# Kernel tuning notes

Measured on AMD Instinct MI355X. Metric: run time of the kernel, lower is better.

Reference implementation:

```python
import jax, jax.numpy as jnp
import numpy as np

N_NODES = 50000
N_EDGES = 600000
VOCAB = 1140
EMB = 10
IN1 = 45   # 35 raw feats + 10 embedding
OUT1 = 128
OUT2 = 64
HID = 32   # LSTM hidden, bidirectional -> 64


def setup_inputs() -> dict:
    key = jax.random.key(0)
    ks = jax.random.split(key, 32)

    def lin(k, out_f, in_f):
        kw, _ = jax.random.split(k)
        return jax.random.normal(kw, (out_f, in_f), jnp.float32) / np.sqrt(in_f), jnp.zeros((out_f,), jnp.float32)

    src = jax.random.randint(ks[0], (N_EDGES,), 0, N_NODES)
    dst = jax.random.randint(ks[1], (N_EDGES,), 0, N_NODES)
    x = jax.random.normal(ks[2], (N_NODES, 35), jnp.float32)
    node_id = jax.random.randint(ks[3], (N_NODES,), 0, VOCAB)

    emb = jax.random.normal(ks[4], (VOCAB, EMB), jnp.float32)
    # dgl GraphConv weights are (in, out)
    convW1 = jax.random.normal(ks[5], (IN1, OUT1), jnp.float32) / np.sqrt(IN1)
    convb1 = jnp.zeros((OUT1,), jnp.float32)
    convW2 = jax.random.normal(ks[6], (OUT1, OUT2), jnp.float32) / np.sqrt(OUT1)
    convb2 = jnp.zeros((OUT2,), jnp.float32)
    bn1g = jnp.ones((OUT1,), jnp.float32); bn1b = jnp.zeros((OUT1,), jnp.float32)
    bn2g = jnp.ones((OUT2,), jnp.float32); bn2b = jnp.zeros((OUT2,), jnp.float32)
    bn3g = jnp.ones((OUT2,), jnp.float32); bn3b = jnp.zeros((OUT2,), jnp.float32)
    sc1W, sc1b = lin(ks[7], OUT1, IN1)
    sc2W, sc2b = lin(ks[8], OUT2, OUT1)
    sc3W, sc3b = lin(ks[9], OUT2, OUT2)
    # torch LSTM layout: W_ih (4H, in), W_hh (4H, H), gate order i,f,g,o
    Wih_f = jax.random.normal(ks[10], (4 * HID, OUT2), jnp.float32) / np.sqrt(OUT2)
    Whh_f = jax.random.normal(ks[11], (4 * HID, HID), jnp.float32) / np.sqrt(HID)
    bih_f = jnp.zeros((4 * HID,), jnp.float32); bhh_f = jnp.zeros((4 * HID,), jnp.float32)
    Wih_b = jax.random.normal(ks[12], (4 * HID, OUT2), jnp.float32) / np.sqrt(OUT2)
    Whh_b = jax.random.normal(ks[13], (4 * HID, HID), jnp.float32) / np.sqrt(HID)
    bih_b = jnp.zeros((4 * HID,), jnp.float32); bhh_b = jnp.zeros((4 * HID,), jnp.float32)
    a1W, a1b = lin(ks[14], OUT2, OUT2)
    a2W, a2b = lin(ks[15], 1, OUT2)
    c1W, c1b = lin(ks[16], OUT2, OUT2)
    c2W, c2b = lin(ks[17], 1, OUT2)

    return dict(src=src, dst=dst, x=x, node_id=node_id, emb=emb,
                convW1=convW1, convb1=convb1, convW2=convW2, convb2=convb2,
                bn1g=bn1g, bn1b=bn1b, bn2g=bn2g, bn2b=bn2b, bn3g=bn3g, bn3b=bn3b,
                sc1W=sc1W, sc1b=sc1b, sc2W=sc2W, sc2b=sc2b, sc3W=sc3W, sc3b=sc3b,
                Wih_f=Wih_f, Whh_f=Whh_f, bih_f=bih_f, bhh_f=bhh_f,
                Wih_b=Wih_b, Whh_b=Whh_b, bih_b=bih_b, bhh_b=bhh_b,
                a1W=a1W, a1b=a1b, a2W=a2W, a2b=a2b, c1W=c1W, c1b=c1b, c2W=c2W, c2b=c2b)


def _lstm_dir(seq, Wih, Whh, bih, bhh):
    # seq: [N, in]; unbatched torch LSTM semantics, one direction
    H = Whh.shape[1]
    pre = seq @ Wih.T + bih + bhh  # [N, 4H], input projection hoisted out of scan

    def step(carry, pt):
        h, c = carry
        g4 = pt + h @ Whh.T
        i, f, g, o = jnp.split(g4, 4)
        i = jax.nn.sigmoid(i); f = jax.nn.sigmoid(f)
        g = jnp.tanh(g); o = jax.nn.sigmoid(o)
        c2 = f * c + i * g
        h2 = o * jnp.tanh(c2)
        return (h2, c2), h2

    init = (jnp.zeros((H,), seq.dtype), jnp.zeros((H,), seq.dtype))
    _, hs = jax.lax.scan(step, init, pre)
    return hs  # [N, H]


def reference(src, dst, x, node_id, emb,
              convW1, convb1, convW2, convb2,
              bn1g, bn1b, bn2g, bn2b, bn3g, bn3b,
              sc1W, sc1b, sc2W, sc2b, sc3W, sc3b,
              Wih_f, Whh_f, bih_f, bhh_f, Wih_b, Whh_b, bih_b, bhh_b,
              a1W, a1b, a2W, a2b, c1W, c1b, c2W, c2b):
    N = x.shape[0]
    # dgl.add_self_loop
    loops = jnp.arange(N)
    s = jnp.concatenate([src, loops])
    d = jnp.concatenate([dst, loops])
    ones = jnp.ones(s.shape, x.dtype)
    deg_out = jax.ops.segment_sum(ones, s, num_segments=N)
    deg_in = jax.ops.segment_sum(ones, d, num_segments=N)
    nrm_out = jax.lax.rsqrt(jnp.maximum(deg_out, 1.0))[:, None]
    nrm_in = jax.lax.rsqrt(jnp.maximum(deg_in, 1.0))[:, None]

    def gconv(h, W, b):
        # GraphConv norm='both': D_in^{-1/2} A D_out^{-1/2} h W + b
        msg = (h * nrm_out)[s]                      # [E+N, F]
        agg = jax.ops.segment_sum(msg, d, num_segments=N)
        return (agg * nrm_in) @ W + b

    def bn(h, g, b):
        mu = h.mean(0)
        var = h.var(0)
        return (h - mu) * jax.lax.rsqrt(var + 1e-5) * g + b

    def linear(h, W, b):
        return h @ W.T + b

    h0 = jnp.concatenate([x, emb[node_id]], axis=1)  # [N, 45]
    x1 = jax.nn.relu(bn(gconv(h0, convW1, convb1), bn1g, bn1b) + linear(h0, sc1W, sc1b))
    x2 = jax.nn.relu(bn(gconv(x1, convW2, convb2), bn2g, bn2b) + linear(x1, sc2W, sc2b))

    hf = _lstm_dir(x2, Wih_f, Whh_f, bih_f, bhh_f)
    hb = _lstm_dir(x2[::-1], Wih_b, Whh_b, bih_b, bhh_b)[::-1]
    x3l = jnp.concatenate([hf, hb], axis=1)          # [N, 64]
    x3 = jax.nn.relu(bn(x3l, bn3g, bn3b) + linear(x2, sc3W, sc3b))

    active = linear(jax.nn.relu(linear(x3, a1W, a1b)), a2W, a2b)
    consume = linear(jax.nn.relu(linear(x3, c1W, c1b)), c2W, c2b)
    return active, consume
```

## Files before the change

kernel.cpp:

```cpp
#include <hip/hip_runtime.h>

#define NN 50000
#define NE 600000
#define CHUNK 100
#define NCH 500
#define WARM 28
#define NB 16
#define SCB 512
#define NSB ((NN + SCB - 1) / SCB)

typedef __attribute__((ext_vector_type(2))) float f2;
typedef __attribute__((ext_vector_type(4))) float f4;

static const size_t OFF_DEG    = 0;
static const size_t OFF_NRM_O  = (size_t)8 * NN;
static const size_t OFF_NRM_I  = (size_t)12 * NN;
static const size_t OFF_STATS  = (size_t)16 * NN;
static const size_t OFF_BSUM   = (size_t)16 * NN + 4096;
static const size_t OFF_BBASE  = (size_t)16 * NN + 8192;
static const size_t OFF_ZONE   = 1048576;
static const size_t OFF_H0   = OFF_ZONE + 0;
static const size_t OFF_X1   = OFF_ZONE + 19200000;
static const size_t OFF_T2   = OFF_ZONE + 44800000;
static const size_t OFF_PRE  = OFF_ZONE + 0;
static const size_t OFF_AGG2 = OFF_ZONE + 57600000;
static const size_t OFF_X2   = OFF_ZONE + 70400000;
static const size_t OFF_X3L  = OFF_ZONE + 83200000;
static const size_t OFF_RP   = OFF_X3L;
static const size_t OFF_CUR  = OFF_X3L + 200016;
static const size_t OFF_CSR  = OFF_X3L + 400032;

__global__ void k_deg(const int* __restrict__ src, const int* __restrict__ dst,
                      int* __restrict__ deg_out, int* __restrict__ deg_in) {
    int e = blockIdx.x * blockDim.x + threadIdx.x;
    if (e < NE) {
        atomicAdd(&deg_out[src[e]], 1);
        atomicAdd(&deg_in[dst[e]], 1);
    }
}

__global__ void __launch_bounds__(512, 1)
k_bsum(const int* __restrict__ deg_in, int* __restrict__ bsum) {
    __shared__ int red[8];
    int b = blockIdx.x, tid = threadIdx.x;
    int n = b * SCB + tid;
    int v = (n < NN) ? deg_in[n] : 0;
    #pragma unroll
    for (int off = 32; off; off >>= 1) v += __shfl_down(v, off);
    if ((tid & 63) == 0) red[tid >> 6] = v;
    __syncthreads();
    if (tid < 8) {
        int s = red[tid];
        #pragma unroll
        for (int off = 4; off; off >>= 1) s += __shfl_down(s, off);
        if (tid == 0) bsum[b] = s;
    }
}

__global__ void k_bscan(const int* __restrict__ bsum, int* __restrict__ bbase) {
    __shared__ int s[128];
    int tid = threadIdx.x;
    int v = (tid < NSB) ? bsum[tid] : 0;
    s[tid] = v;
    __syncthreads();
    for (int off = 1; off < 128; off <<= 1) {
        int t = 0;
        if (tid >= off) t = s[tid - off];
        __syncthreads();
        if (tid >= off) s[tid] += t;
        __syncthreads();
    }
    if (tid < NSB) bbase[tid] = (tid == 0) ? 0 : s[tid - 1];
    if (tid == 0) bbase[NSB] = s[127];
}

__global__ void __launch_bounds__(512, 1)
k_rfill(const int* __restrict__ deg_in, const int* __restrict__ bbase,
        int* __restrict__ rowptr, int* __restrict__ cursor) {
    __shared__ int s[SCB];
    int b = blockIdx.x, tid = threadIdx.x;
    int n = b * SCB + tid;
    int v = (n < NN) ? deg_in[n] : 0;
    s[tid] = v;
    __syncthreads();
    for (int off = 1; off < SCB; off <<= 1) {
        int t = 0;
        if (tid >= off) t = s[tid - off];
        __syncthreads();
        if (tid >= off) s[tid] += t;
        __syncthreads();
    }
    if (n < NN) {
        rowptr[n] = bbase[b] + s[tid] - v;
        cursor[n] = 0;
    }
    if (n == NN - 1) rowptr[NN] = bbase[NSB];
}

__global__ void k_fill(const int* __restrict__ src, const int* __restrict__ dst,
                       const int* __restrict__ rowptr, int* __restrict__ cursor,
                       int* __restrict__ csr) {
    int e = blockIdx.x * blockDim.x + threadIdx.x;
    if (e >= NE) return;
    int d = dst[e];
    int idx = atomicAdd(&cursor[d], 1);
    csr[rowptr[d] + idx] = src[e];
}

__global__ void k_h0(const float* __restrict__ x, const int* __restrict__ nid,
                     const float* __restrict__ emb,
                     const int* __restrict__ deg_out, const int* __restrict__ deg_in,
                     float* __restrict__ nrm_out, float* __restrict__ nrm_in,
                     float* __restrict__ h0) {
    int n = blockIdx.x * blockDim.x + threadIdx.x;
    if (n >= NN) return;
    nrm_out[n] = rsqrtf((float)(deg_out[n] + 1));
    nrm_in[n]  = rsqrtf((float)(deg_in[n] + 1));
    const float* xr = x + (size_t)n * 35;
    float* hr = h0 + (size_t)n * 48;
    #pragma unroll
    for (int k = 0; k < 35; k++) hr[k] = xr[k];
    const float* er = emb + (size_t)nid[n] * 10;
    #pragma unroll
    for (int k = 0; k < 10; k++) hr[35 + k] = er[k];
    hr[45] = 0.f; hr[46] = 0.f; hr[47] = 0.f;
}

__global__ void __launch_bounds__(256, 1)
k_gy1(const int* __restrict__ csr, const int* __restrict__ rowptr,
      const float* __restrict__ h0, const float* __restrict__ nrm_out,
      const float* __restrict__ nrm_in, const float* __restrict__ W1,
      const float* __restrict__ b1, float* __restrict__ y1) {
    __shared__ float vs[NB * 48];
    int n0 = blockIdx.x * NB, t = threadIdx.x;
    int w = t >> 6, lane = t & 63;
    #pragma unroll
    for (int i = 0; i < 4; i++) {
        int n = w * 4 + i;
        int gn = n0 + n;
        int e0 = rowptr[gn], e1 = rowptr[gn + 1];
        float acc = 0.f;
        #pragma unroll 4
        for (int e = e0; e < e1; e++) {
            int s = csr[e];
            if (lane < 48) acc += h0[(size_t)s * 48 + lane] * nrm_out[s];
        }
        if (lane < 48)
            vs[n * 48 + lane] = (acc + h0[(size_t)gn * 48 + lane] * nrm_out[gn]) * nrm_in[gn];
    }
    __syncthreads();
    int j = t & 127, p = t >> 7;
    float wr[45];
    #pragma unroll
    for (int k = 0; k < 45; k++) wr[k] = W1[k * 128 + j];
    float bj = b1[j];
    #pragma unroll
    for (int i = 0; i < NB / 2; i++) {
        int n = p + 2 * i;
        float acc = bj;
        #pragma unroll
        for (int k = 0; k < 45; k++) acc += vs[n * 48 + k] * wr[k];
        y1[(size_t)(n0 + n) * 128 + j] = acc;
    }
}

template<int F>
__global__ void k_red(const float* __restrict__ y, float* __restrict__ stats) {
    const int parts = 256 / F;
    __shared__ float s1[256], s2[256];
    int tid = threadIdx.x;
    int o = tid % F, p = tid / F;
    float a = 0.f, b = 0.f;
    int n0 = blockIdx.x * 512;
    int n1 = n0 + 512; if (n1 > NN) n1 = NN;
    for (int n = n0 + p; n < n1; n += parts) {
        float v = y[(size_t)n * F + o];
        a += v; b += v * v;
    }
    s1[tid] = a; s2[tid] = b;
    __syncthreads();
    if (p == 0) {
        #pragma unroll
        for (int pp = 1; pp < parts; pp++) { a += s1[pp * F + o]; b += s2[pp * F + o]; }
        atomicAdd(&stats[o], a);
        atomicAdd(&stats[F + o], b);
    }
}

__global__ void __launch_bounds__(256, 1)
k_x1t2(const float* __restrict__ h0, const float* __restrict__ sc1W,
       const float* __restrict__ sc1b, const float* __restrict__ g,
       const float* __restrict__ bb, const float* __restrict__ stats,
       const float* __restrict__ W2, const float* __restrict__ nrm_out,
       float* __restrict__ y1x1, float* __restrict__ t2) {
    __shared__ float hs[NB * 48];
    __shared__ float xs1[NB * 128];
    int n0 = blockIdx.x * NB, t = threadIdx.x;
    for (int i = t; i < NB * 48; i += 256) hs[i] = h0[(size_t)n0 * 48 + i];
    __syncthreads();
    {
        int j = t & 127, p = t >> 7;
        float w[45];
        #pragma unroll
        for (int k = 0; k < 45; k++) w[k] = sc1W[j * 45 + k];
        float mu = stats[j] * (1.f / NN);
        float var = stats[128 + j] * (1.f / NN) - mu * mu;
        float istd = rsqrtf(var + 1e-5f);
        float gj = g[j], bbj = bb[j], sbj = sc1b[j];
        #pragma unroll
        for (int i = 0; i < NB / 2; i++) {
            int n = p + 2 * i;
            float acc = sbj;
            #pragma unroll
            for (int k = 0; k < 45; k++) acc += hs[n * 48 + k] * w[k];
            size_t idx = (size_t)(n0 + n) * 128 + j;
            float v = (y1x1[idx] - mu) * istd * gj + bbj + acc;
            v = v > 0.f ? v : 0.f;
            y1x1[idx] = v;
            xs1[n * 128 + j] = v;
        }
    }
    __syncthreads();
    {
        int j = t & 63, p = t >> 6;
        float w[128];
        #pragma unroll
        for (int k = 0; k < 128; k++) w[k] = W2[k * 64 + j];
        #pragma unroll
        for (int i = 0; i < 4; i++) {
            int n = p + 4 * i;
            const f4* xv = (const f4*)(xs1 + n * 128);
            float acc = 0.f;
            #pragma unroll
            for (int m = 0; m < 32; m++) {
                f4 h = xv[m];
                acc += h.x * w[4 * m] + h.y * w[4 * m + 1] + h.z * w[4 * m + 2] + h.w * w[4 * m + 3];
            }
            t2[(size_t)(n0 + n) * 64 + j] = acc * nrm_out[n0 + n];
        }
    }
}

__global__ void k_gather2(const int* __restrict__ csr, const int* __restrict__ rowptr,
                          const float* __restrict__ t2, const float* __restrict__ nrm_in,
                          const float* __restrict__ b2, float* __restrict__ y2) {
    int n = blockIdx.x * 4 + (threadIdx.x >> 6);
    int lane = threadIdx.x & 63;
    if (n >= NN) return;
    int e0 = rowptr[n], e1 = rowptr[n + 1];
    float acc = t2[(size_t)n * 64 + lane];
    #pragma unroll 4
    for (int e = e0; e < e1; e++) {
        int s = csr[e];
        acc += t2[(size_t)s * 64 + lane];
    }
    y2[(size_t)n * 64 + lane] = acc * nrm_in[n] + b2[lane];
}

__global__ void __launch_bounds__(256, 1)
k_x2b(const float* __restrict__ x1, const float* __restrict__ y2,
      const float* __restrict__ sc2W, const float* __restrict__ sc2b,
      const float* __restrict__ g, const float* __restrict__ bb,
      const float* __restrict__ stats, float* __restrict__ x2) {
    __shared__ float xs[NB * 128];
    int n0 = blockIdx.x * NB, t = threadIdx.x;
    ((f4*)xs)[t] = ((const f4*)(x1 + (size_t)n0 * 128))[t];
    ((f4*)xs)[t + 256] = ((const f4*)(x1 + (size_t)n0 * 128))[t + 256];
    __syncthreads();
    int j = t & 63, p = t >> 6;
    float w[128];
    #pragma unroll
    for (int k = 0; k < 128; k++) w[k] = sc2W[j * 128 + k];
    float mu = stats[j] * (1.f / NN);
    float var = stats[64 + j] * (1.f / NN) - mu * mu;
    float istd = rsqrtf(var + 1e-5f);
    float gj = g[j], bbj = bb[j], sbj = sc2b[j];
    #pragma unroll
    for (int i = 0; i < 4; i++) {
        int n = p + 4 * i;
        const f4* xv = (const f4*)(xs + n * 128);
        float acc = sbj;
        #pragma unroll
        for (int m = 0; m < 32; m++) {
            f4 h = xv[m];
            acc += h.x * w[4 * m] + h.y * w[4 * m + 1] + h.z * w[4 * m + 2] + h.w * w[4 * m + 3];
        }
        size_t idx = (size_t)(n0 + n) * 64 + j;
        float v = (y2[idx] - mu) * istd * gj + bbj + acc;
        x2[idx] = v > 0.f ? v : 0.f;
    }
}

__global__ void k_preb(const float* __restrict__ x2,
                       const float* __restrict__ Wf, const float* __restrict__ bif, const float* __restrict__ bhf,
                       const float* __restrict__ Wb, const float* __restrict__ bib, const float* __restrict__ bhb,
                       float* __restrict__ pre) {
    __shared__ float xs[NB * 64];
    int n0 = blockIdx.x * NB, t = threadIdx.x;
    ((f4*)xs)[t] = ((const f4*)(x2 + (size_t)n0 * 64))[t];
    __syncthreads();
    int dir = t >> 7, jj = t & 127;
    const float* __restrict__ W = dir ? Wb : Wf;
    float w[64];
    #pragma unroll
    for (int k = 0; k < 64; k++) w[k] = W[jj * 64 + k];
    float bias = dir ? (bib[jj] + bhb[jj]) : (bif[jj] + bhf[jj]);
    #pragma unroll
    for (int n = 0; n < NB; n++) {
        const f4* xv = (const f4*)(xs + n * 64);
        float acc = bias;
        #pragma unroll
        for (int m = 0; m < 16; m++) {
            f4 h = xv[m];
            acc += h.x * w[4 * m] + h.y * w[4 * m + 1] + h.z * w[4 * m + 2] + h.w * w[4 * m + 3];
        }
        pre[((size_t)dir * NN + n0 + n) * 128 + jj] = acc;
    }
}

__global__ void __launch_bounds__(64, 1)
k_lstm5(const float* __restrict__ pre, const float* __restrict__ Whh_f,
        const float* __restrict__ Whh_b, float* __restrict__ x3l) {
    const int dir = blockIdx.x / NCH;
    const int ci  = blockIdx.x % NCH;
    const int c0  = ci * CHUNK;
    const int s_start = (c0 >= WARM) ? (c0 - WARM) : 0;
    const int c_end   = c0 + CHUNK;

    const float* __restrict__ P = pre + (size_t)dir * NN * 128;
    const float* __restrict__ Whh = dir ? Whh_b : Whh_f;
    const int lane = threadIdx.x;
    const int j = lane & 31;
    const bool lower = lane < 32;

    __shared__ f4 hbuf[2][8];

    f2 wa[16], wb[16];
    #pragma unroll
    for (int m = 0; m < 16; m++) {
        wa[m] = ((const f2*)(Whh + (size_t)lane * 32))[m];
        wb[m] = ((const f2*)(Whh + (size_t)(lane + 64) * 32))[m];
    }

    if (lower) ((float*)hbuf[0])[j] = 0.f;
    float c = 0.f;

    float pa[8], pb[8], nxa[8], nxb[8];
    #pragma unroll
    for (int k = 0; k < 8; k++) {
        int s = s_start + k;
        int t = dir ? (NN - 1 - s) : s;
        pa[k] = P[(size_t)t * 128 + lane];
        pb[k] = P[(size_t)t * 128 + 64 + lane];
    }

    for (int base = s_start; base < c_end; base += 8) {
        int nxt = (base + 8 < c_end) ? base + 8 : base;
        #pragma unroll
        for (int k = 0; k < 8; k++) {
            int s = nxt + k;
            int t = dir ? (NN - 1 - s) : s;
            nxa[k] = P[(size_t)t * 128 + lane];
            nxb[k] = P[(size_t)t * 128 + 64 + lane];
        }
        #pragma unroll
        for (int k = 0; k < 8; k++) {
            const int s = base + k;
            const int b = s & 1;
            f2 a0 = {0.f, 0.f}, a1 = {0.f, 0.f};
            f2 b0 = {0.f, 0.f}, b1 = {0.f, 0.f};
            #pragma unroll
            for (int m = 0; m < 8; m++) {
                f4 hv = hbuf[b][m];
                f2 hlo = hv.xy, hhi = hv.zw;
                a0 += wa[2 * m] * hlo;
                a1 += wa[2 * m + 1] * hhi;
                b0 += wb[2 * m] * hlo;
                b1 += wb[2 * m + 1] * hhi;
            }
            f2 ra = a0 + a1, rb = b0 + b1;
            float ga = pa[k] + ra.x + ra.y;
            float gb = pb[k] + rb.x + rb.y;
            float act_a = 1.f / (1.f + __expf(-ga));
            float eb = __expf(lower ? -2.f * gb : -gb);
            float sb = 1.f / (1.f + eb);
            float act_b = lower ? 2.f * sb - 1.f : sb;
            float u = act_a * act_b;
            float xu = __shfl_xor(u, 32);
            c = act_a * c + xu;
            float th = 2.f / (1.f + __expf(-2.f * c)) - 1.f;
            float h = act_b * th;
            if (!lower) {
                ((float*)hbuf[b ^ 1])[j] = h;
                if (s >= c0 && s < c_end) {
                    int t = dir ? (NN - 1 - s) : s;
                    x3l[(size_t)t * 64 + dir * 32 + j] = h;
                }
            }
        }
        #pragma unroll
        for (int k = 0; k < 8; k++) { pa[k] = nxa[k]; pb[k] = nxb[k]; }
    }
}

__global__ void __launch_bounds__(256, 1)
k_x3h(const float* __restrict__ x2, const float* __restrict__ sc3W,
      const float* __restrict__ sc3b, const float* __restrict__ g,
      const float* __restrict__ bb, const float* __restrict__ stats,
      const float* __restrict__ x3l,
      const float* __restrict__ a1W, const float* __restrict__ a1b,
      const float* __restrict__ a2W, const float* __restrict__ a2b,
      const float* __restrict__ c1W, const float* __restrict__ c1b,
      const float* __restrict__ c2W, const float* __restrict__ c2b,
      float* __restrict__ outp) {
    __shared__ float xs[NB * 64];
    __shared__ float xs3[NB * 64];
    __shared__ float prod[2][NB][64];
    int n0 = blockIdx.x * NB, t = threadIdx.x;
    ((f4*)xs)[t] = ((const f4*)(x2 + (size_t)n0 * 64))[t];
    __syncthreads();
    {
        int j = t & 63, p = t >> 6;
        float w[64];
        #pragma unroll
        for (int k = 0; k < 64; k++) w[k] = sc3W[j * 64 + k];
        float mu = stats[j] * (1.f / NN);
        float var = stats[64 + j] * (1.f / NN) - mu * mu;
        float istd = rsqrtf(var + 1e-5f);
        float gj = g[j], bbj = bb[j], sbj = sc3b[j];
        #pragma unroll
        for (int i = 0; i < 4; i++) {
            int n = p + 4 * i;
            const f4* xv = (const f4*)(xs + n * 64);
            float acc = sbj;
            #pragma unroll
            for (int m = 0; m < 16; m++) {
                f4 h = xv[m];
                acc += h.x * w[4 * m] + h.y * w[4 * m + 1] + h.z * w[4 * m + 2] + h.w * w[4 * m + 3];
            }
            float v = (x3l[(size_t)(n0 + n) * 64 + j] - mu) * istd * gj + bbj + acc;
            xs3[n * 64 + j] = v > 0.f ? v : 0.f;
        }
    }
    __syncthreads();
    {
        int hd = t >> 7, p = (t >> 6) & 1, j = t & 63;
        const float* __restrict__ W1h = hd ? c1W : a1W;
        const float* __restrict__ b1h = hd ? c1b : a1b;
        const float* __restrict__ w2h = hd ? c2W : a2W;
        float w[64];
        #pragma unroll
        for (int k = 0; k < 64; k++) w[k] = W1h[j * 64 + k];
        float b1j = b1h[j], w2j = w2h[j];
        #pragma unroll
        for (int i = 0; i < NB / 2; i++) {
            int n = p + 2 * i;
            const f4* xv = (const f4*)(xs3 + n * 64);
            float acc = b1j;
            #pragma unroll
            for (int m = 0; m < 16; m++) {
                f4 h = xv[m];
                acc += h.x * w[4 * m] + h.y * w[4 * m + 1] + h.z * w[4 * m + 2] + h.w * w[4 * m + 3];
            }
            prod[hd][n][j] = (acc > 0.f ? acc : 0.f) * w2j;
        }
    }
    __syncthreads();
    if (t < 32) {
        int hd2 = t >> 4, n = t & 15;
        float s = 0.f;
        #pragma unroll
        for (int k = 0; k < 64; k++) s += prod[hd2][n][k];
        outp[(size_t)hd2 * NN + n0 + n] = s + (hd2 ? c2b[0] : a2b[0]);
    }
}

extern "C" void kernel_launch(void* const* d_in, const int* in_sizes, int n_in,
                              void* d_out, int out_size, void* d_ws, size_t ws_size,
                              hipStream_t stream) {
    const int*   src   = (const int*)  d_in[0];
    const int*   dst   = (const int*)  d_in[1];
    const float* x     = (const float*)d_in[2];
    const int*   nid   = (const int*)  d_in[3];
    const float* emb   = (const float*)d_in[4];
    const float* W1    = (const float*)d_in[5];
    const float* b1    = (const float*)d_in[6];
    const float* W2    = (const float*)d_in[7];
    const float* b2    = (const float*)d_in[8];
    const float* bn1g  = (const float*)d_in[9];
    const float* bn1b  = (const float*)d_in[10];
    const float* bn2g  = (const float*)d_in[11];
    const float* bn2b  = (const float*)d_in[12];
    const float* bn3g  = (const float*)d_in[13];
    const float* bn3b  = (const float*)d_in[14];
    const float* sc1W  = (const float*)d_in[15];
    const float* sc1b  = (const float*)d_in[16];
    const float* sc2W  = (const float*)d_in[17];
    const float* sc2b  = (const float*)d_in[18];
    const float* sc3W  = (const float*)d_in[19];
    const float* sc3b  = (const float*)d_in[20];
    const float* Wih_f = (const float*)d_in[21];
    const float* Whh_f = (const float*)d_in[22];
    const float* bih_f = (const float*)d_in[23];
    const float* bhh_f = (const float*)d_in[24];
    const float* Wih_b = (const float*)d_in[25];
    const float* Whh_b = (const float*)d_in[26];
    const float* bih_b = (const float*)d_in[27];
    const float* bhh_b = (const float*)d_in[28];
    const float* a1W   = (const float*)d_in[29];
    const float* a1b   = (const float*)d_in[30];
    const float* a2W   = (const float*)d_in[31];
    const float* a2b   = (const float*)d_in[32];
    const float* c1W   = (const float*)d_in[33];
    const float* c1b   = (const float*)d_in[34];
    const float* c2W   = (const float*)d_in[35];
    const float* c2b   = (const float*)d_in[36];
    float* outp = (float*)d_out;
    char* ws = (char*)d_ws;

    int*   deg_out = (int*)  (ws + OFF_DEG);
    int*   deg_in  = (int*)  (ws + OFF_DEG + 4 * (size_t)NN);
    float* nrm_out = (float*)(ws + OFF_NRM_O);
    float* nrm_in  = (float*)(ws + OFF_NRM_I);
    float* stats   = (float*)(ws + OFF_STATS);
    int*   bsum    = (int*)  (ws + OFF_BSUM);
    int*   bbase   = (int*)  (ws + OFF_BBASE);
    float* h0   = (float*)(ws + OFF_H0);
    float* x1   = (float*)(ws + OFF_X1);
    float* t2   = (float*)(ws + OFF_T2);
    float* pre  = (float*)(ws + OFF_PRE);
    float* y2   = (float*)(ws + OFF_AGG2);
    float* x2   = (float*)(ws + OFF_X2);
    float* x3l  = (float*)(ws + OFF_X3L);
    int*   rowptr = (int*)(ws + OFF_RP);
    int*   cursor = (int*)(ws + OFF_CUR);
    int*   csr    = (int*)(ws + OFF_CSR);

    hipMemsetAsync(ws + OFF_DEG, 0, 8 * (size_t)NN, stream);
    hipMemsetAsync(ws + OFF_STATS, 0, 512 * 4, stream);

    k_deg<<<(NE + 255) / 256, 256, 0, stream>>>(src, dst, deg_out, deg_in);
    k_bsum<<<NSB, 512, 0, stream>>>(deg_in, bsum);
    k_bscan<<<1, 128, 0, stream>>>(bsum, bbase);
    k_rfill<<<NSB, 512, 0, stream>>>(deg_in, bbase, rowptr, cursor);
    k_fill<<<(NE + 255) / 256, 256, 0, stream>>>(src, dst, rowptr, cursor, csr);
    k_h0<<<(NN + 255) / 256, 256, 0, stream>>>(x, nid, emb, deg_out, deg_in, nrm_out, nrm_in, h0);
    k_gy1<<<NN / NB, 256, 0, stream>>>(csr, rowptr, h0, nrm_out, nrm_in, W1, b1, x1);
    k_red<128><<<(NN + 511) / 512, 256, 0, stream>>>(x1, stats);
    k_x1t2<<<NN / NB, 256, 0, stream>>>(h0, sc1W, sc1b, bn1g, bn1b, stats, W2, nrm_out, x1, t2);
    k_gather2<<<(NN + 3) / 4, 256, 0, stream>>>(csr, rowptr, t2, nrm_in, b2, y2);
    k_red<64><<<(NN + 511) / 512, 256, 0, stream>>>(y2, stats + 256);
    k_x2b<<<NN / NB, 256, 0, stream>>>(x1, y2, sc2W, sc2b, bn2g, bn2b, stats + 256, x2);
    k_preb<<<NN / NB, 256, 0, stream>>>(x2, Wih_f, bih_f, bhh_f, Wih_b, bih_b, bhh_b, pre);
    k_lstm5<<<2 * NCH, 64, 0, stream>>>(pre, Whh_f, Whh_b, x3l);
    k_red<64><<<(NN + 511) / 512, 256, 0, stream>>>(x3l, stats + 384);
    k_x3h<<<NN / NB, 256, 0, stream>>>(x2, sc3W, sc3b, bn3g, bn3b, stats + 384, x3l,
                                       a1W, a1b, a2W, a2b, c1W, c1b, c2W, c2b, outp);
}
```

Before: 610.2 us.

## Pre-scale h0 by out-norm and use one wave per node in gathers

k_h0 now also writes a copy of h0 already multiplied by nrm_out. This removes the per-edge nrm_out load and multiply from the layer-1 gather. k_gy1 and the layer-2 gather now run 1024-thread blocks with one 64-lane wave per destination node, instead of each wave serially walking four nodes, which exposes more parallel edge walks. This costs an extra 9.6MB write of the scaled copy, and the large blocks with launch_bounds(1024,1) may limit occupancy and register use in the 45-weight matmul phase.

```diff
diff --git a/kernel.cpp b/kernel.cpp
--- a/kernel.cpp
+++ b/kernel.cpp
@@ -20,6 +20,7 @@
 static const size_t OFF_BBASE  = (size_t)16 * NN + 8192;
 static const size_t OFF_ZONE   = 1048576;
 static const size_t OFF_H0   = OFF_ZONE + 0;
+static const size_t OFF_H0S  = OFF_ZONE + 9600000;
 static const size_t OFF_X1   = OFF_ZONE + 19200000;
 static const size_t OFF_T2   = OFF_ZONE + 44800000;
 static const size_t OFF_PRE  = OFF_ZONE + 0;
@@ -111,43 +112,42 @@
                      const float* __restrict__ emb,
                      const int* __restrict__ deg_out, const int* __restrict__ deg_in,
                      float* __restrict__ nrm_out, float* __restrict__ nrm_in,
-                     float* __restrict__ h0) {
+                     float* __restrict__ h0, float* __restrict__ h0s) {
     int n = blockIdx.x * blockDim.x + threadIdx.x;
     if (n >= NN) return;
-    nrm_out[n] = rsqrtf((float)(deg_out[n] + 1));
+    float no = rsqrtf((float)(deg_out[n] + 1));
+    nrm_out[n] = no;
     nrm_in[n]  = rsqrtf((float)(deg_in[n] + 1));
     const float* xr = x + (size_t)n * 35;
     float* hr = h0 + (size_t)n * 48;
-    #pragma unroll
-    for (int k = 0; k < 35; k++) hr[k] = xr[k];
+    float* hsr = h0s + (size_t)n * 48;
+    #pragma unroll
+    for (int k = 0; k < 35; k++) { float v = xr[k]; hr[k] = v; hsr[k] = v * no; }
     const float* er = emb + (size_t)nid[n] * 10;
     #pragma unroll
-    for (int k = 0; k < 10; k++) hr[35 + k] = er[k];
+    for (int k = 0; k < 10; k++) { float v = er[k]; hr[35 + k] = v; hsr[35 + k] = v * no; }
     hr[45] = 0.f; hr[46] = 0.f; hr[47] = 0.f;
-}
-
-__global__ void __launch_bounds__(256, 1)
+    hsr[45] = 0.f; hsr[46] = 0.f; hsr[47] = 0.f;
+}
+
+__global__ void __launch_bounds__(1024, 1)
 k_gy1(const int* __restrict__ csr, const int* __restrict__ rowptr,
-      const float* __restrict__ h0, const float* __restrict__ nrm_out,
-      const float* __restrict__ nrm_in, const float* __restrict__ W1,
-      const float* __restrict__ b1, float* __restrict__ y1) {
+      const float* __restrict__ h0s, const float* __restrict__ nrm_in,
+      const float* __restrict__ W1, const float* __restrict__ b1,
+      float* __restrict__ y1) {
     __shared__ float vs[NB * 48];
     int n0 = blockIdx.x * NB, t = threadIdx.x;
     int w = t >> 6, lane = t & 63;
-    #pragma unroll
-    for (int i = 0; i < 4; i++) {
-        int n = w * 4 + i;
-        int gn = n0 + n;
-        int e0 = rowptr[gn], e1 = rowptr[gn + 1];
-        float acc = 0.f;
-        #pragma unroll 4
-        for (int e = e0; e < e1; e++) {
-            int s = csr[e];
-            if (lane < 48) acc += h0[(size_t)s * 48 + lane] * nrm_out[s];
-        }
-        if (lane < 48)
-            vs[n * 48 + lane] = (acc + h0[(size_t)gn * 48 + lane] * nrm_out[gn]) * nrm_in[gn];
-    }
+    int gn = n0 + w;
+    int e0 = rowptr[gn], e1 = rowptr[gn + 1];
+    float acc = 0.f;
+    #pragma unroll 8
+    for (int e = e0; e < e1; e++) {
+        int s = csr[e];
+        if (lane < 48) acc += h0s[(size_t)s * 48 + lane];
+    }
+    if (lane < 48)
+        vs[w * 48 + lane] = (acc + h0s[(size_t)gn * 48 + lane]) * nrm_in[gn];
     __syncthreads();
     int j = t & 127, p = t >> 7;
     float wr[45];
@@ -155,12 +155,12 @@
     for (int k = 0; k < 45; k++) wr[k] = W1[k * 128 + j];
     float bj = b1[j];
     #pragma unroll
-    for (int i = 0; i < NB / 2; i++) {
-        int n = p + 2 * i;
-        float acc = bj;
-        #pragma unroll
-        for (int k = 0; k < 45; k++) acc += vs[n * 48 + k] * wr[k];
-        y1[(size_t)(n0 + n) * 128 + j] = acc;
+    for (int i = 0; i < 2; i++) {
+        int n = p + 8 * i;
+        float a = bj;
+        #pragma unroll
+        for (int k = 0; k < 45; k++) a += vs[n * 48 + k] * wr[k];
+        y1[(size_t)(n0 + n) * 128 + j] = a;
     }
 }
 
@@ -241,15 +241,16 @@
     }
 }
 
-__global__ void k_gather2(const int* __restrict__ csr, const int* __restrict__ rowptr,
-                          const float* __restrict__ t2, const float* __restrict__ nrm_in,
-                          const float* __restrict__ b2, float* __restrict__ y2) {
-    int n = blockIdx.x * 4 + (threadIdx.x >> 6);
-    int lane = threadIdx.x & 63;
-    if (n >= NN) return;
+__global__ void __launch_bounds__(1024, 1)
+k_g2(const int* __restrict__ csr, const int* __restrict__ rowptr,
+     const float* __restrict__ t2, const float* __restrict__ nrm_in,
+     const float* __restrict__ b2, float* __restrict__ y2) {
+    int t = threadIdx.x;
+    int w = t >> 6, lane = t & 63;
+    int n = blockIdx.x * NB + w;
     int e0 = rowptr[n], e1 = rowptr[n + 1];
     float acc = t2[(size_t)n * 64 + lane];
-    #pragma unroll 4
+    #pragma unroll 8
     for (int e = e0; e < e1; e++) {
         int s = csr[e];
         acc += t2[(size_t)s * 64 + lane];
@@ -526,6 +527,7 @@
     int*   bsum    = (int*)  (ws + OFF_BSUM);
     int*   bbase   = (int*)  (ws + OFF_BBASE);
     float* h0   = (float*)(ws + OFF_H0);
+    float* h0s  = (float*)(ws + OFF_H0S);
     float* x1   = (float*)(ws + OFF_X1);
     float* t2   = (float*)(ws + OFF_T2);
     float* pre  = (float*)(ws + OFF_PRE);
@@ -544,11 +546,11 @@
     k_bscan<<<1, 128, 0, stream>>>(bsum, bbase);
     k_rfill<<<NSB, 512, 0, stream>>>(deg_in, bbase, rowptr, cursor);
     k_fill<<<(NE + 255) / 256, 256, 0, stream>>>(src, dst, rowptr, cursor, csr);
-    k_h0<<<(NN + 255) / 256, 256, 0, stream>>>(x, nid, emb, deg_out, deg_in, nrm_out, nrm_in, h0);
-    k_gy1<<<NN / NB, 256, 0, stream>>>(csr, rowptr, h0, nrm_out, nrm_in, W1, b1, x1);
+    k_h0<<<(NN + 255) / 256, 256, 0, stream>>>(x, nid, emb, deg_out, deg_in, nrm_out, nrm_in, h0, h0s);
+    k_gy1<<<NN / NB, 1024, 0, stream>>>(csr, rowptr, h0s, nrm_in, W1, b1, x1);
     k_red<128><<<(NN + 511) / 512, 256, 0, stream>>>(x1, stats);
     k_x1t2<<<NN / NB, 256, 0, stream>>>(h0, sc1W, sc1b, bn1g, bn1b, stats, W2, nrm_out, x1, t2);
-    k_gather2<<<(NN + 3) / 4, 256, 0, stream>>>(csr, rowptr, t2, nrm_in, b2, y2);
+    k_g2<<<NN / NB, 1024, 0, stream>>>(csr, rowptr, t2, nrm_in, b2, y2);
     k_red<64><<<(NN + 511) / 512, 256, 0, stream>>>(y2, stats + 256);
     k_x2b<<<NN / NB, 256, 0, stream>>>(x1, y2, sc2W, sc2b, bn2g, bn2b, stats + 256, x2);
     k_preb<<<NN / NB, 256, 0, stream>>>(x2, Wih_f, bih_f, bhh_f, Wih_b, bih_b, bhh_b, pre);
```

Result: slower. 678.8 us (+11.2%).
